# Performance work log

Hardware: AMD Instinct MI355X
Metric: run time of the kernel (lower is better)

## Reference

```python
import jax, jax.numpy as jnp
import numpy as np

BN_EPS = 1e-5


def _bn_relu(h, gamma, beta):
    # BatchNorm1d in training mode: normalize over (batch, length) per channel
    mean = h.mean(axis=(0, 2), keepdims=True)
    var = h.var(axis=(0, 2), keepdims=True)
    h = (h - mean) * jax.lax.rsqrt(var + BN_EPS)
    h = h * gamma[None, :, None] + beta[None, :, None]
    return jax.nn.relu(h)


def _gather(ldesc, idx):
    # ldesc: [B, D, N], idx: [B, M] -> [B, D, M]
    B, D, N = ldesc.shape
    M = idx.shape[1]
    return jnp.take_along_axis(ldesc, jnp.broadcast_to(idx[:, None, :], (B, D, M)), axis=2)


def _scatter_mean(src, idx, N):
    # per-batch scatter-mean: src [B, D, M], idx [B, M] -> [B, D, N]
    def one(s, i):
        D = s.shape[0]
        sums = jnp.zeros((D, N), s.dtype).at[:, i].add(s)
        cnts = jnp.zeros((N,), s.dtype).at[i].add(1.0)
        return sums / jnp.maximum(cnts, 1.0)[None, :]
    return jax.vmap(one)(src, idx)


def _endpoint_update(ldesc, line_enc, idx, W1, b1, g1, bt1, W2, b2):
    B, D, _ = ldesc.shape
    ld = _gather(ldesc, idx)                                   # [B, D, 2L]
    # flip endpoint pairs: neighbor endpoint of each endpoint
    neigh = ld.reshape(B, D, -1, 2)[..., ::-1].reshape(B, D, -1)
    msg = jnp.concatenate([ld, neigh, line_enc], axis=1)       # [B, 3D, 2L]
    h = jnp.einsum('oc,bcm->bom', W1, msg) + b1[None, :, None]  # Conv1d k=1
    h = _bn_relu(h, g1, bt1)
    out = jnp.einsum('oc,bcm->bom', W2, h) + b2[None, :, None]
    return out                                                  # [B, D, 2L]


def setup_inputs() -> dict:
    key = jax.random.key(0)
    ks = jax.random.split(key, 12)
    B, D, N, M = 8, 256, 8192, 8192
    inp = {
        'ldesc0': jax.random.normal(ks[0], (B, D, N), jnp.float32),
        'ldesc1': jax.random.normal(ks[1], (B, D, N), jnp.float32),
        'line_enc0': jax.random.normal(ks[2], (B, D, M), jnp.float32),
        'line_enc1': jax.random.normal(ks[3], (B, D, M), jnp.float32),
        'lines_junc_idx0': jax.random.randint(ks[4], (B, M), 0, N),
        'lines_junc_idx1': jax.random.randint(ks[5], (B, M), 0, N),
        'W1': jax.random.normal(ks[6], (2 * D, 3 * D), jnp.float32) * (1.0 / np.sqrt(3 * D)),
        'b1': jnp.zeros((2 * D,), jnp.float32),
        'g1': jnp.ones((2 * D,), jnp.float32),
        'bt1': jnp.zeros((2 * D,), jnp.float32),
        'W2': jax.random.normal(ks[7], (D, 2 * D), jnp.float32) * (1.0 / np.sqrt(2 * D)),
        'b2': jnp.zeros((D,), jnp.float32),
    }
    return inp


def reference(ldesc0, ldesc1, line_enc0, line_enc1, lines_junc_idx0, lines_junc_idx1,
              W1, b1, g1, bt1, W2, b2):
    N = ldesc0.shape[2]
    up0 = _endpoint_update(ldesc0, line_enc0, lines_junc_idx0, W1, b1, g1, bt1, W2, b2)
    up1 = _endpoint_update(ldesc1, line_enc1, lines_junc_idx1, W1, b1, g1, bt1, W2, b2)
    out0 = ldesc0 + _scatter_mean(up0, lines_junc_idx0, N)
    out1 = ldesc1 + _scatter_mean(up1, lines_junc_idx1, N)
    return (out0, out1)
```

## Files before the change

### kernel.cpp

```cpp
#include <hip/hip_runtime.h>
#include <hip/hip_bf16.h>

#define B_  8
#define D_  256
#define N_  8192
#define M_  8192
#define O1_ 512
#define K1_ 768
#define K2_ 512

typedef unsigned short u16;
typedef __attribute__((ext_vector_type(8))) short bf8;
typedef __attribute__((ext_vector_type(4))) float f4;

static __device__ __forceinline__ float bf2f(u16 u) {
    unsigned v = ((unsigned)u) << 16;
    return __uint_as_float(v);
}
static __device__ __forceinline__ u16 f2bf(float f) {
    __hip_bfloat16 h = __float2bfloat16(f);
    return *reinterpret_cast<u16*>(&h);
}
static __device__ __forceinline__ void gl_lds16(const u16* g, u16* l) {
    __builtin_amdgcn_global_load_lds((const __attribute__((address_space(1))) void*)g,
                                     (__attribute__((address_space(3))) void*)l, 16, 0, 0);
}
static __device__ __forceinline__ int swz64(int r) {
    return (((r >> 1) & 1) << 4) | (((r >> 2) & 1) << 5);
}

__global__ __launch_bounds__(256) void k_transpose_bf16(const float* __restrict__ src,
                                                        u16* __restrict__ dst, int R, int C) {
    __shared__ float t[32][33];
    const int b  = blockIdx.z;
    const int c0 = blockIdx.x * 32, r0 = blockIdx.y * 32;
    const int tx = threadIdx.x, ty = threadIdx.y;
    const float* s = src + (size_t)b * R * C;
    u16* d = dst + (size_t)b * C * R;
#pragma unroll
    for (int i = 0; i < 4; ++i) {
        int r = r0 + ty + i * 8;
        t[ty + i * 8][tx] = s[(size_t)r * C + (c0 + tx)];
    }
    __syncthreads();
#pragma unroll
    for (int i = 0; i < 4; ++i) {
        int c = c0 + ty + i * 8;
        d[(size_t)c * R + (r0 + tx)] = f2bf(t[tx][ty + i * 8]);
    }
}

__global__ __launch_bounds__(256) void k_convert_w(const float* __restrict__ W1, const float* __restrict__ W2,
                                                   u16* __restrict__ W1b, u16* __restrict__ W2b) {
    int i = blockIdx.x * 256 + threadIdx.x;
    const int n1 = O1_ * K1_;
    const int n2 = D_ * K2_;
    if (i < n1) W1b[i] = f2bf(W1[i]);
    int j = i - n1;
    if (j >= 0 && j < n2) W2b[j] = f2bf(W2[j]);
}

#define NT1 24
__global__ __launch_bounds__(512, 2) void k_gemm1(const u16* __restrict__ W1b,
                                                  const u16* __restrict__ Tld,
                                                  const u16* __restrict__ Tle,
                                                  const int* __restrict__ idx,
                                                  u16* __restrict__ hbuf) {
    __shared__ u16 LA[4][256 * 32];
    __shared__ u16 LB[4][256 * 32];
    const int b  = blockIdx.z;
    const int o0 = blockIdx.y * 256;
    const int m0 = blockIdx.x * 256;
    const int tid = threadIdx.x;
    const int w = tid >> 6, l = tid & 63;
    const int wr = w >> 2;
    const int wcn = w & 3;

    const int srow   = tid >> 2;
    const int scol16 = (tid & 3) * 16;

    int na[2], nb[2], mrow[2];
    const u16* aSrc[2];
    int bcol[2];
#pragma unroll
    for (int j = 0; j < 2; ++j) {
        int r = srow + j * 128;
        int m = m0 + r;
        mrow[j] = m;
        na[j] = idx[b * M_ + m];
        nb[j] = idx[b * M_ + (m ^ 1)];
        int sw = swz64(r);
        aSrc[j] = W1b + (size_t)(o0 + r) * K1_ + ((scol16 ^ sw) >> 1);
        bcol[j] = (scol16 ^ sw) >> 1;
    }

    int ar[8], br[4];
#pragma unroll
    for (int i = 0; i < 8; ++i) {
        int r = wr * 128 + i * 16 + (l & 15);
        ar[i] = r * 32 + ((((l >> 4) * 16) ^ swz64(r)) >> 1);
    }
#pragma unroll
    for (int j = 0; j < 4; ++j) {
        int r = wcn * 64 + j * 16 + (l & 15);
        br[j] = r * 32 + ((((l >> 4) * 16) ^ swz64(r)) >> 1);
    }

#define STAGE1(kt, buf)                                                              \
    {                                                                                \
        const int seg = (kt) >> 3;                                                   \
        const int off = ((kt) & 7) * 32;                                             \
        _Pragma("unroll")                                                            \
        for (int j = 0; j < 2; ++j)                                                  \
            gl_lds16(aSrc[j] + (kt) * 32, &LA[buf][j * 4096 + tid * 8]);             \
        _Pragma("unroll")                                                            \
        for (int j = 0; j < 2; ++j) {                                                \
            const u16* s;                                                            \
            if (seg == 0)      s = Tld + (size_t)(b * N_ + na[j]) * D_ + off + bcol[j]; \
            else if (seg == 1) s = Tld + (size_t)(b * N_ + nb[j]) * D_ + off + bcol[j]; \
            else               s = Tle + (size_t)(b * M_ + mrow[j]) * D_ + off + bcol[j]; \
            gl_lds16(s, &LB[buf][j * 4096 + tid * 8]);                               \
        }                                                                            \
    }

    f4 acc[8][4];
#pragma unroll
    for (int i = 0; i < 8; ++i)
#pragma unroll
        for (int j = 0; j < 4; ++j) acc[i][j] = {0.f, 0.f, 0.f, 0.f};

    STAGE1(0, 0);
    STAGE1(1, 1);
    STAGE1(2, 2);
    asm volatile("s_waitcnt vmcnt(8)" ::: "memory");
    __builtin_amdgcn_s_barrier();
    __builtin_amdgcn_sched_barrier(0);

    for (int t = 0; t < NT1; ++t) {
        const int buf = t & 3;
        if (t + 3 < NT1) STAGE1(t + 3, (t + 3) & 3);

        bf8 aF[8], bF[4];
#pragma unroll
        for (int i = 0; i < 8; ++i) aF[i] = *reinterpret_cast<const bf8*>(&LA[buf][ar[i]]);
#pragma unroll
        for (int j = 0; j < 4; ++j) bF[j] = *reinterpret_cast<const bf8*>(&LB[buf][br[j]]);

        __builtin_amdgcn_s_setprio(1);
#pragma unroll
        for (int i = 0; i < 8; ++i)
#pragma unroll
            for (int j = 0; j < 4; ++j)
                acc[i][j] = __builtin_amdgcn_mfma_f32_16x16x32_bf16(aF[i], bF[j], acc[i][j], 0, 0, 0);
        __builtin_amdgcn_s_setprio(0);

        if (t <= NT1 - 4)      asm volatile("s_waitcnt vmcnt(8)" ::: "memory");
        else if (t == NT1 - 3) asm volatile("s_waitcnt vmcnt(4)" ::: "memory");
        else                   asm volatile("s_waitcnt vmcnt(0)" ::: "memory");
        __builtin_amdgcn_s_barrier();
        __builtin_amdgcn_sched_barrier(0);
    }
#undef STAGE1

#pragma unroll
    for (int j = 0; j < 4; ++j) {
        int m = m0 + wcn * 64 + j * 16 + (l & 15);
        size_t rowbase = (size_t)(b * M_ + m) * O1_;
#pragma unroll
        for (int i = 0; i < 8; ++i) {
            int orow = o0 + wr * 128 + i * 16 + (l >> 4) * 4;
            ushort4 pk;
            pk.x = f2bf(acc[i][j].x);
            pk.y = f2bf(acc[i][j].y);
            pk.z = f2bf(acc[i][j].z);
            pk.w = f2bf(acc[i][j].w);
            *reinterpret_cast<ushort4*>(&hbuf[rowbase + orow]) = pk;
        }
    }
}

__global__ __launch_bounds__(256) void k_stats(const u16* __restrict__ hbuf, float* __restrict__ stats) {
    const int t = threadIdx.x;
    const size_t row0 = (size_t)blockIdx.x * 256;
    float s0 = 0.f, q0 = 0.f, s1 = 0.f, q1 = 0.f;
    for (int r = 0; r < 256; ++r) {
        const u16* p = hbuf + (row0 + r) * O1_;
        float v0 = bf2f(p[t]);
        float v1 = bf2f(p[t + 256]);
        s0 += v0; q0 += v0 * v0;
        s1 += v1; q1 += v1 * v1;
    }
    atomicAdd(&stats[t], s0);
    atomicAdd(&stats[O1_ + t], q0);
    atomicAdd(&stats[t + 256], s1);
    atomicAdd(&stats[O1_ + t + 256], q1);
}

__global__ void k_finalize_ac(const float* __restrict__ stats, const float* __restrict__ g1,
                              const float* __restrict__ bt1, float* __restrict__ ac) {
    int o = blockIdx.x * 256 + threadIdx.x;
    if (o >= O1_) return;
    const float inv = 1.0f / ((float)B_ * (float)M_);
    float mean = stats[o] * inv;
    float var  = stats[O1_ + o] * inv - mean * mean;
    var = fmaxf(var, 0.0f);
    float a = g1[o] * rsqrtf(var + 1e-5f);
    ac[o] = a;
    ac[O1_ + o] = bt1[o] - mean * a;
}

__global__ void k_count_int(const int* __restrict__ idx, int* __restrict__ cnt) {
    int i = blockIdx.x * 256 + threadIdx.x;
    if (i < B_ * M_) atomicAdd(&cnt[(i >> 13) * N_ + idx[i]], 1);
}

__global__ __launch_bounds__(1024) void k_scan(const int* __restrict__ cnt, int* __restrict__ offs,
                                               int* __restrict__ fill) {
    __shared__ int wsum[1024];
    const int b = blockIdx.x;
    const int t = threadIdx.x;
    const int base = b * N_;
    int v[8]; int s = 0;
#pragma unroll
    for (int k = 0; k < 8; ++k) { v[k] = cnt[base + t * 8 + k]; s += v[k]; }
    wsum[t] = s;
    __syncthreads();
    for (int off = 1; off < 1024; off <<= 1) {
        int add = (t >= off) ? wsum[t - off] : 0;
        __syncthreads();
        wsum[t] += add;
        __syncthreads();
    }
    int run = (t > 0) ? wsum[t - 1] : 0;
#pragma unroll
    for (int k = 0; k < 8; ++k) {
        offs[base + t * 8 + k] = run;
        fill[base + t * 8 + k] = run;
        run += v[k];
    }
}

__global__ void k_fill(const int* __restrict__ idx, int* __restrict__ fill, int* __restrict__ mlist) {
    int i = blockIdx.x * 256 + threadIdx.x;
    if (i < B_ * M_) {
        int b = i >> 13, m = i & (M_ - 1);
        int pos = atomicAdd(&fill[b * N_ + idx[i]], 1);
        mlist[(size_t)b * M_ + pos] = m;
    }
}

__global__ __launch_bounds__(256) void k_gemm2(const u16* __restrict__ W2b,
                                               const u16* __restrict__ hbuf,
                                               const float* __restrict__ ac,
                                               const float* __restrict__ b2,
                                               u16* __restrict__ up) {
    __shared__ u16 At[128 * 32];
    __shared__ u16 Bt[128 * 32];
    __shared__ float acs[1024];
    const int b  = blockIdx.z;
    const int d0 = blockIdx.y * 128;
    const int m0 = blockIdx.x * 128;
    const int tid = threadIdx.x;
    const int w = tid >> 6, l = tid & 63;
    const int lr = l >> 2, lc = (l & 3) * 8;

    acs[tid]       = ac[tid];
    acs[tid + 256] = ac[tid + 256];
    acs[tid + 512] = ac[tid + 512];
    acs[tid + 768] = ac[tid + 768];

    const u16* pA[2]; const u16* pB[2];
#pragma unroll
    for (int t = 0; t < 2; ++t) {
        int row = t * 64 + w * 16 + lr;
        pA[t] = W2b + (size_t)(d0 + row) * K2_ + lc;
        int m  = m0 + row;
        pB[t] = hbuf + (size_t)(b * M_ + m) * O1_ + lc;
    }
    const int wr = w >> 1, wc = w & 1;
    f4 acc[4][4];
#pragma unroll
    for (int i = 0; i < 4; ++i)
#pragma unroll
        for (int j = 0; j < 4; ++j) acc[i][j] = {0.f, 0.f, 0.f, 0.f};

    const int aoff = (wr * 64 + (l & 15)) * 32 + (l >> 4) * 8;
    const int boff = (wc * 64 + (l & 15)) * 32 + (l >> 4) * 8;
    const int bdst = (w * 16 + lr) * 32 + lc;

    __syncthreads();

    for (int kk = 0; kk < 16; ++kk) {
        const int o = kk * 32 + lc;
        f4 A0 = *reinterpret_cast<const f4*>(&acs[o]);
        f4 A1 = *reinterpret_cast<const f4*>(&acs[o + 4]);
        f4 C0 = *reinterpret_cast<const f4*>(&acs[512 + o]);
        f4 C1 = *reinterpret_cast<const f4*>(&acs[512 + o + 4]);
#pragma unroll
        for (int t = 0; t < 2; ++t) {
            gl_lds16(pA[t] + kk * 32, At + (t * 64 + w * 16) * 32);
            const ushort4* ps = reinterpret_cast<const ushort4*>(pB[t] + kk * 32);
            ushort4 v0 = ps[0], v1 = ps[1];
            union { ushort4 u4[2]; bf8 v8; } pk;
            pk.u4[0].x = f2bf(fmaxf(bf2f(v0.x) * A0.x + C0.x, 0.0f));
            pk.u4[0].y = f2bf(fmaxf(bf2f(v0.y) * A0.y + C0.y, 0.0f));
            pk.u4[0].z = f2bf(fmaxf(bf2f(v0.z) * A0.z + C0.z, 0.0f));
            pk.u4[0].w = f2bf(fmaxf(bf2f(v0.w) * A0.w + C0.w, 0.0f));
            pk.u4[1].x = f2bf(fmaxf(bf2f(v1.x) * A1.x + C1.x, 0.0f));
            pk.u4[1].y = f2bf(fmaxf(bf2f(v1.y) * A1.y + C1.y, 0.0f));
            pk.u4[1].z = f2bf(fmaxf(bf2f(v1.z) * A1.z + C1.z, 0.0f));
            pk.u4[1].w = f2bf(fmaxf(bf2f(v1.w) * A1.w + C1.w, 0.0f));
            *reinterpret_cast<bf8*>(&Bt[t * 64 * 32 + bdst]) = pk.v8;
        }
        __syncthreads();
        bf8 aF[4], bF[4];
#pragma unroll
        for (int i = 0; i < 4; ++i) aF[i] = *reinterpret_cast<const bf8*>(&At[aoff + i * 16 * 32]);
#pragma unroll
        for (int j = 0; j < 4; ++j) bF[j] = *reinterpret_cast<const bf8*>(&Bt[boff + j * 16 * 32]);
#pragma unroll
        for (int i = 0; i < 4; ++i)
#pragma unroll
            for (int j = 0; j < 4; ++j)
                acc[i][j] = __builtin_amdgcn_mfma_f32_16x16x32_bf16(aF[i], bF[j], acc[i][j], 0, 0, 0);
        __syncthreads();
    }

#pragma unroll
    for (int j = 0; j < 4; ++j) {
        int m = m0 + wc * 64 + j * 16 + (l & 15);
        size_t rowbase = (size_t)(b * M_ + m) * D_;
#pragma unroll
        for (int i = 0; i < 4; ++i) {
            int d = d0 + wr * 64 + i * 16 + (l >> 4) * 4;
            ushort4 pk;
            pk.x = f2bf(acc[i][j].x + b2[d + 0]);
            pk.y = f2bf(acc[i][j].y + b2[d + 1]);
            pk.z = f2bf(acc[i][j].z + b2[d + 2]);
            pk.w = f2bf(acc[i][j].w + b2[d + 3]);
            *reinterpret_cast<ushort4*>(&up[rowbase + d]) = pk;
        }
    }
}

__global__ __launch_bounds__(256) void k_reduce_finalize(const float* __restrict__ ldesc,
                                                         const u16* __restrict__ up,
                                                         const int* __restrict__ cnt,
                                                         const int* __restrict__ offs,
                                                         const int* __restrict__ mlist,
                                                         float* __restrict__ out) {
    __shared__ float lds[32][257];
    const int b  = blockIdx.z;
    const int n0 = blockIdx.x * 32;
    const int tx = threadIdx.x, ty = threadIdx.y;
#pragma unroll
    for (int i = 0; i < 4; ++i) {
        int nl = ty + i * 8;
        int n  = n0 + nl;
        int c   = cnt[b * N_ + n];
        int off = offs[b * N_ + n];
        float inv = 1.0f / (float)max(c, 1);
        float acc[8] = {0.f, 0.f, 0.f, 0.f, 0.f, 0.f, 0.f, 0.f};
        for (int e = 0; e < c; ++e) {
            int m = mlist[(size_t)b * M_ + off + e];
            const ushort4* row = reinterpret_cast<const ushort4*>(up + (size_t)(b * M_ + m) * D_ + tx * 8);
            ushort4 aa = row[0], bb = row[1];
            acc[0] += bf2f(aa.x); acc[1] += bf2f(aa.y); acc[2] += bf2f(aa.z); acc[3] += bf2f(aa.w);
            acc[4] += bf2f(bb.x); acc[5] += bf2f(bb.y); acc[6] += bf2f(bb.z); acc[7] += bf2f(bb.w);
        }
#pragma unroll
        for (int k = 0; k < 8; ++k) lds[nl][tx * 8 + k] = acc[k] * inv;
    }
    __syncthreads();
#pragma unroll
    for (int i = 0; i < 32; ++i) {
        int d = ty + i * 8;
        size_t o2 = (size_t)(b * D_ + d) * N_ + n0 + tx;
        out[o2] = ldesc[o2] + lds[tx][d];
    }
}

__global__ void k_marker(float* out, float v) { out[0] = v; }

extern "C" void kernel_launch(void* const* d_in, const int* in_sizes, int n_in,
                              void* d_out, int out_size, void* d_ws, size_t ws_size,
                              hipStream_t stream) {
    const float* ldesc0 = (const float*)d_in[0];
    const float* ldesc1 = (const float*)d_in[1];
    const float* le0    = (const float*)d_in[2];
    const float* le1    = (const float*)d_in[3];
    const int*   idx0   = (const int*)d_in[4];
    const int*   idx1   = (const int*)d_in[5];
    const float* W1     = (const float*)d_in[6];
    const float* g1     = (const float*)d_in[8];
    const float* bt1    = (const float*)d_in[9];
    const float* W2     = (const float*)d_in[10];
    const float* b2     = (const float*)d_in[11];
    float* out = (float*)d_out;

    char* ws = (char*)d_ws;
    const size_t oTld   = 0;
    const size_t oTle   = 33554432;
    const size_t oH     = 67108864;
    const size_t oW1b   = 134217728;
    const size_t oW2b   = oW1b + 786432;
    const size_t oStats = oW2b + 262144;
    const size_t oAC    = oStats + 4096;
    const size_t NEED   = oAC + 4096;
    if (ws_size < NEED) {
        k_marker<<<1, 1, 0, stream>>>(out, 1000.0f + (float)(ws_size >> 20));
        return;
    }
    u16*   Tld   = (u16*)(ws + oTld);
    u16*   up    = (u16*)(ws + oTld);
    u16*   Tle   = (u16*)(ws + oTle);
    int*   cnt   = (int*)(ws + oTle);
    int*   offs  = (int*)(ws + oTle + 262144);
    int*   fill  = (int*)(ws + oTle + 524288);
    int*   mlist = (int*)(ws + oTle + 786432);
    u16*   hbuf  = (u16*)(ws + oH);
    u16*   W1b   = (u16*)(ws + oW1b);
    u16*   W2b   = (u16*)(ws + oW2b);
    float* stats = (float*)(ws + oStats);
    float* ac    = (float*)(ws + oAC);

    k_convert_w<<<2048, 256, 0, stream>>>(W1, W2, W1b, W2b);

    const dim3 tb(32, 8);
    for (int s = 0; s < 2; ++s) {
        const float* ld  = s ? ldesc1 : ldesc0;
        const float* le  = s ? le1 : le0;
        const int*   idx = s ? idx1 : idx0;
        float* outp = out + (size_t)s * B_ * D_ * N_;

        k_transpose_bf16<<<dim3(N_ / 32, D_ / 32, B_), tb, 0, stream>>>(ld, Tld, D_, N_);
        k_transpose_bf16<<<dim3(M_ / 32, D_ / 32, B_), tb, 0, stream>>>(le, Tle, D_, M_);
        k_gemm1<<<dim3(M_ / 256, O1_ / 256, B_), 512, 0, stream>>>(W1b, Tld, Tle, idx, hbuf);
        hipMemsetAsync(stats, 0, 4096, stream);
        k_stats<<<256, 256, 0, stream>>>(hbuf, stats);
        k_finalize_ac<<<2, 256, 0, stream>>>(stats, g1, bt1, ac);
        hipMemsetAsync(cnt, 0, (size_t)B_ * N_ * 4, stream);
        k_count_int<<<B_ * M_ / 256, 256, 0, stream>>>(idx, cnt);
        k_scan<<<B_, 1024, 0, stream>>>(cnt, offs, fill);
        k_fill<<<B_ * M_ / 256, 256, 0, stream>>>(idx, fill, mlist);
        k_gemm2<<<dim3(M_ / 128, D_ / 128, B_), 256, 0, stream>>>(W2b, hbuf, ac, b2, up);
        k_reduce_finalize<<<dim3(N_ / 32, 1, B_), tb, 0, stream>>>(ld, up, cnt, offs, mlist, outp);
    }
}
```

Baseline: 485.0 us.

## Shrink GEMM1 tiles, widen transpose tiles, and split stats reduction over more blocks

GEMM1 moves from a 256x256 tile with 512 threads and a 4-stage LDS pipeline to a 128x128 tile with 256 threads and 3 stages, which gives 4x as many blocks and sets launch bounds to 3 blocks per CU. The transpose kernel now uses 64x64 tiles with a 64x4 thread layout, and the stats kernel reduces 32 rows per block instead of 256, so far more blocks take part. The aim is better occupancy and parallelism across the CUs. The trade-off is less data reuse per GEMM tile and many more atomic adds in the stats step.

```diff
diff --git a/kernel.cpp b/kernel.cpp
--- a/kernel.cpp
+++ b/kernel.cpp
@@ -31,22 +31,22 @@
 
 __global__ __launch_bounds__(256) void k_transpose_bf16(const float* __restrict__ src,
                                                         u16* __restrict__ dst, int R, int C) {
-    __shared__ float t[32][33];
+    __shared__ float t[64][65];
     const int b  = blockIdx.z;
-    const int c0 = blockIdx.x * 32, r0 = blockIdx.y * 32;
+    const int c0 = blockIdx.x * 64, r0 = blockIdx.y * 64;
     const int tx = threadIdx.x, ty = threadIdx.y;
     const float* s = src + (size_t)b * R * C;
     u16* d = dst + (size_t)b * C * R;
 #pragma unroll
-    for (int i = 0; i < 4; ++i) {
-        int r = r0 + ty + i * 8;
-        t[ty + i * 8][tx] = s[(size_t)r * C + (c0 + tx)];
+    for (int i = 0; i < 16; ++i) {
+        int r = r0 + ty + i * 4;
+        t[ty + i * 4][tx] = s[(size_t)r * C + (c0 + tx)];
     }
     __syncthreads();
 #pragma unroll
-    for (int i = 0; i < 4; ++i) {
-        int c = c0 + ty + i * 8;
-        d[(size_t)c * R + (r0 + tx)] = f2bf(t[tx][ty + i * 8]);
+    for (int i = 0; i < 16; ++i) {
+        int c = c0 + ty + i * 4;
+        d[(size_t)c * R + (r0 + tx)] = f2bf(t[tx][ty + i * 4]);
     }
 }
 
@@ -61,32 +61,31 @@
 }
 
 #define NT1 24
-__global__ __launch_bounds__(512, 2) void k_gemm1(const u16* __restrict__ W1b,
+__global__ __launch_bounds__(256, 3) void k_gemm1(const u16* __restrict__ W1b,
                                                   const u16* __restrict__ Tld,
                                                   const u16* __restrict__ Tle,
                                                   const int* __restrict__ idx,
                                                   u16* __restrict__ hbuf) {
-    __shared__ u16 LA[4][256 * 32];
-    __shared__ u16 LB[4][256 * 32];
+    __shared__ u16 LA[3][128 * 32];
+    __shared__ u16 LB[3][128 * 32];
     const int b  = blockIdx.z;
-    const int o0 = blockIdx.y * 256;
-    const int m0 = blockIdx.x * 256;
+    const int o0 = blockIdx.y * 128;
+    const int m0 = blockIdx.x * 128;
     const int tid = threadIdx.x;
     const int w = tid >> 6, l = tid & 63;
-    const int wr = w >> 2;
-    const int wcn = w & 3;
+    const int wr = w >> 1, wc = w & 1;
 
     const int srow   = tid >> 2;
     const int scol16 = (tid & 3) * 16;
 
-    int na[2], nb[2], mrow[2];
+    int na[2], nb[2], mm[2];
     const u16* aSrc[2];
     int bcol[2];
 #pragma unroll
     for (int j = 0; j < 2; ++j) {
-        int r = srow + j * 128;
+        int r = j * 64 + srow;
         int m = m0 + r;
-        mrow[j] = m;
+        mm[j] = m;
         na[j] = idx[b * M_ + m];
         nb[j] = idx[b * M_ + (m ^ 1)];
         int sw = swz64(r);
@@ -94,69 +93,67 @@
         bcol[j] = (scol16 ^ sw) >> 1;
     }
 
-    int ar[8], br[4];
-#pragma unroll
-    for (int i = 0; i < 8; ++i) {
-        int r = wr * 128 + i * 16 + (l & 15);
+    int ar[4], br[4];
+#pragma unroll
+    for (int i = 0; i < 4; ++i) {
+        int r = wr * 64 + i * 16 + (l & 15);
         ar[i] = r * 32 + ((((l >> 4) * 16) ^ swz64(r)) >> 1);
     }
 #pragma unroll
     for (int j = 0; j < 4; ++j) {
-        int r = wcn * 64 + j * 16 + (l & 15);
+        int r = wc * 64 + j * 16 + (l & 15);
         br[j] = r * 32 + ((((l >> 4) * 16) ^ swz64(r)) >> 1);
     }
 
-#define STAGE1(kt, buf)                                                              \
-    {                                                                                \
-        const int seg = (kt) >> 3;                                                   \
-        const int off = ((kt) & 7) * 32;                                             \
-        _Pragma("unroll")                                                            \
-        for (int j = 0; j < 2; ++j)                                                  \
-            gl_lds16(aSrc[j] + (kt) * 32, &LA[buf][j * 4096 + tid * 8]);             \
-        _Pragma("unroll")                                                            \
-        for (int j = 0; j < 2; ++j) {                                                \
-            const u16* s;                                                            \
+#define STAGE1(kt, buf)                                                                 \
+    {                                                                                   \
+        const int seg = (kt) >> 3;                                                      \
+        const int off = ((kt) & 7) * 32;                                                \
+        _Pragma("unroll")                                                               \
+        for (int j = 0; j < 2; ++j)                                                     \
+            gl_lds16(aSrc[j] + (kt) * 32, &LA[buf][j * 2048 + tid * 8]);                \
+        _Pragma("unroll")                                                               \
+        for (int j = 0; j < 2; ++j) {                                                   \
+            const u16* s;                                                               \
             if (seg == 0)      s = Tld + (size_t)(b * N_ + na[j]) * D_ + off + bcol[j]; \
             else if (seg == 1) s = Tld + (size_t)(b * N_ + nb[j]) * D_ + off + bcol[j]; \
-            else               s = Tle + (size_t)(b * M_ + mrow[j]) * D_ + off + bcol[j]; \
-            gl_lds16(s, &LB[buf][j * 4096 + tid * 8]);                               \
-        }                                                                            \
-    }
-
-    f4 acc[8][4];
-#pragma unroll
-    for (int i = 0; i < 8; ++i)
+            else               s = Tle + (size_t)(b * M_ + mm[j]) * D_ + off + bcol[j]; \
+            gl_lds16(s, &LB[buf][j * 2048 + tid * 8]);                                  \
+        }                                                                               \
+    }
+
+    f4 acc[4][4];
+#pragma unroll
+    for (int i = 0; i < 4; ++i)
 #pragma unroll
         for (int j = 0; j < 4; ++j) acc[i][j] = {0.f, 0.f, 0.f, 0.f};
 
     STAGE1(0, 0);
     STAGE1(1, 1);
-    STAGE1(2, 2);
-    asm volatile("s_waitcnt vmcnt(8)" ::: "memory");
+    asm volatile("s_waitcnt vmcnt(4)" ::: "memory");
     __builtin_amdgcn_s_barrier();
     __builtin_amdgcn_sched_barrier(0);
 
     for (int t = 0; t < NT1; ++t) {
-        const int buf = t & 3;
-        if (t + 3 < NT1) STAGE1(t + 3, (t + 3) & 3);
-
-        bf8 aF[8], bF[4];
-#pragma unroll
-        for (int i = 0; i < 8; ++i) aF[i] = *reinterpret_cast<const bf8*>(&LA[buf][ar[i]]);
+        const int buf = t % 3;
+        if (t + 2 < NT1) STAGE1(t + 2, (t + 2) % 3);
+
+        bf8 aF[4], bF[4];
+#pragma unroll
+        for (int i = 0; i < 4; ++i) aF[i] = *reinterpret_cast<const bf8*>(&LA[buf][ar[i]]);
 #pragma unroll
         for (int j = 0; j < 4; ++j) bF[j] = *reinterpret_cast<const bf8*>(&LB[buf][br[j]]);
 
         __builtin_amdgcn_s_setprio(1);
 #pragma unroll
-        for (int i = 0; i < 8; ++i)
+        for (int i = 0; i < 4; ++i)
 #pragma unroll
             for (int j = 0; j < 4; ++j)
                 acc[i][j] = __builtin_amdgcn_mfma_f32_16x16x32_bf16(aF[i], bF[j], acc[i][j], 0, 0, 0);
         __builtin_amdgcn_s_setprio(0);
 
-        if (t <= NT1 - 4)      asm volatile("s_waitcnt vmcnt(8)" ::: "memory");
-        else if (t == NT1 - 3) asm volatile("s_waitcnt vmcnt(4)" ::: "memory");
-        else                   asm volatile("s_waitcnt vmcnt(0)" ::: "memory");
+        if (t < NT1 - 2) asm volatile("s_waitcnt vmcnt(4)" ::: "memory");
+        else             asm volatile("s_waitcnt vmcnt(0)" ::: "memory");
         __builtin_amdgcn_s_barrier();
         __builtin_amdgcn_sched_barrier(0);
     }
@@ -164,11 +161,11 @@
 
 #pragma unroll
     for (int j = 0; j < 4; ++j) {
-        int m = m0 + wcn * 64 + j * 16 + (l & 15);
+        int m = m0 + wc * 64 + j * 16 + (l & 15);
         size_t rowbase = (size_t)(b * M_ + m) * O1_;
 #pragma unroll
-        for (int i = 0; i < 8; ++i) {
-            int orow = o0 + wr * 128 + i * 16 + (l >> 4) * 4;
+        for (int i = 0; i < 4; ++i) {
+            int orow = o0 + wr * 64 + i * 16 + (l >> 4) * 4;
             ushort4 pk;
             pk.x = f2bf(acc[i][j].x);
             pk.y = f2bf(acc[i][j].y);
@@ -181,9 +178,9 @@
 
 __global__ __launch_bounds__(256) void k_stats(const u16* __restrict__ hbuf, float* __restrict__ stats) {
     const int t = threadIdx.x;
-    const size_t row0 = (size_t)blockIdx.x * 256;
+    const size_t row0 = (size_t)blockIdx.x * 32;
     float s0 = 0.f, q0 = 0.f, s1 = 0.f, q1 = 0.f;
-    for (int r = 0; r < 256; ++r) {
+    for (int r = 0; r < 32; ++r) {
         const u16* p = hbuf + (row0 + r) * O1_;
         float v0 = bf2f(p[t]);
         float v1 = bf2f(p[t + 256]);
@@ -426,6 +423,7 @@
 
     k_convert_w<<<2048, 256, 0, stream>>>(W1, W2, W1b, W2b);
 
+    const dim3 tb64(64, 4);
     const dim3 tb(32, 8);
     for (int s = 0; s < 2; ++s) {
         const float* ld  = s ? ldesc1 : ldesc0;
@@ -433,11 +431,11 @@
         const int*   idx = s ? idx1 : idx0;
         float* outp = out + (size_t)s * B_ * D_ * N_;
 
-        k_transpose_bf16<<<dim3(N_ / 32, D_ / 32, B_), tb, 0, stream>>>(ld, Tld, D_, N_);
-        k_transpose_bf16<<<dim3(M_ / 32, D_ / 32, B_), tb, 0, stream>>>(le, Tle, D_, M_);
-        k_gemm1<<<dim3(M_ / 256, O1_ / 256, B_), 512, 0, stream>>>(W1b, Tld, Tle, idx, hbuf);
+        k_transpose_bf16<<<dim3(N_ / 64, D_ / 64, B_), tb64, 0, stream>>>(ld, Tld, D_, N_);
+        k_transpose_bf16<<<dim3(M_ / 64, D_ / 64, B_), tb64, 0, stream>>>(le, Tle, D_, M_);
+        k_gemm1<<<dim3(M_ / 128, O1_ / 128, B_), 256, 0, stream>>>(W1b, Tld, Tle, idx, hbuf);
         hipMemsetAsync(stats, 0, 4096, stream);
-        k_stats<<<256, 256, 0, stream>>>(hbuf, stats);
+        k_stats<<<B_ * M_ / 32, 256, 0, stream>>>(hbuf, stats);
         k_finalize_ac<<<2, 256, 0, stream>>>(stats, g1, bt1, ac);
         hipMemsetAsync(cnt, 0, (size_t)B_ * N_ * 4, stream);
         k_count_int<<<B_ * M_ / 256, 256, 0, stream>>>(idx, cnt);
```

After: 538.9 us. 11.1% more time.
